# Performance work log

Measured on AMD Instinct MI355X. Metric: run time of the kernel, lower is better.

## Reference

```python
import jax, jax.numpy as jnp
import numpy as np

MARGIN = 40.0


def setup_inputs() -> dict:
    key = jax.random.key(0)
    k1, k2 = jax.random.split(key)
    feat = jax.random.normal(k1, (4096, 512), dtype=jnp.float32)
    targets = jax.random.randint(k2, (4096,), 0, 64, dtype=jnp.int64)
    return {"feat": feat, "targets": targets}


def reference(feat, targets):
    # corr: (n, n) Gram matrix of features
    corr = feat @ feat.T
    # mask[i, j] = True if same class
    mask = targets[:, None] == targets[None, :]
    big = jnp.asarray(jnp.finfo(corr.dtype).max, corr.dtype)
    # per-row min over positives, max over negatives
    corr_ap = jnp.min(jnp.where(mask, corr, big), axis=1)
    corr_an = jnp.max(jnp.where(mask, -big, corr), axis=1)
    # MarginRankingLoss(margin=40) with y = 1: mean(relu(-(ap - an) + margin))
    loss = jnp.mean(jax.nn.relu(corr_an - corr_ap + MARGIN))
    return loss
```

## Files before the change

kernel.cpp:

```cpp
#include <hip/hip_runtime.h>
#include <float.h>
#include <stdint.h>


#define N_ROWS 4096
#define D_K    512
#define BT     64
#define BK     32
#define NTB    (N_ROWS / BT)
#define NTILES (NTB * (NTB + 1) / 2)
#define MARGIN 40.0f
#define FOLD_BLOCKS 16

typedef __bf16 bf16_t;
typedef bf16_t bf16x8 __attribute__((ext_vector_type(8)));
typedef float  floatx4 __attribute__((ext_vector_type(4)));
typedef unsigned short ushort_t;
typedef ushort_t ushortx8 __attribute__((ext_vector_type(8)));

#define GLOAD_LDS16(g, l)                                        \
    __builtin_amdgcn_global_load_lds(                            \
        (const __attribute__((address_space(1))) void*)(g),      \
        (__attribute__((address_space(3))) void*)(l), 16, 0, 0)

__device__ __forceinline__ ushort_t f2bf_rne(float x) {
    uint32_t u = __builtin_bit_cast(uint32_t, x);
    return (ushort_t)((u + 0x7FFFu + ((u >> 16) & 1u)) >> 16);
}

__global__ __launch_bounds__(256) void cast_kernel(
    const float* __restrict__ f, ushort_t* __restrict__ o,
    int* __restrict__ counter)
{
    const int gid = blockIdx.x * 256 + threadIdx.x;
    if (gid == 0) *counter = 0;

    const int i = gid * 8;
    const float4 v0 = *(const float4*)(f + i);
    const float4 v1 = *(const float4*)(f + i + 4);
    ushortx8 r;
    r[0] = f2bf_rne(v0.x); r[1] = f2bf_rne(v0.y);
    r[2] = f2bf_rne(v0.z); r[3] = f2bf_rne(v0.w);
    r[4] = f2bf_rne(v1.x); r[5] = f2bf_rne(v1.y);
    r[6] = f2bf_rne(v1.z); r[7] = f2bf_rne(v1.w);
    *(ushortx8*)(o + i) = r;
}

__global__ __launch_bounds__(256) void gram_mfma_kernel(
    const ushort_t* __restrict__ fb, const int* __restrict__ tgt,
    float* __restrict__ ap_part, float* __restrict__ an_part)
{
    __shared__ __align__(16) ushort_t As[BT * BK];
    __shared__ __align__(16) ushort_t Bs[BT * BK];
    __shared__ int tgI[BT];
    __shared__ int tgJ[BT];
    __shared__ float apRed[2][BT],  anRed[2][BT];
    __shared__ float apRedT[2][BT], anRedT[2][BT];

    int bi = 0, rem = blockIdx.x;
    while (rem >= NTB - bi) { rem -= NTB - bi; ++bi; }
    const int bj = bi + rem;

    const int tid  = threadIdx.x;
    const int i0   = bi * BT;
    const int j0   = bj * BT;
    const int lane = tid & 63;
    const int wave = tid >> 6;
    const int wr   = wave >> 1;
    const int wc   = wave & 1;
    const int lr   = lane & 15;
    const int lg   = lane >> 4;

    if (tid < BT)            tgI[tid]      = tgt[i0 + tid];
    else if (tid < 2 * BT)   tgJ[tid - BT] = tgt[j0 + tid - BT];

    const int srow = tid >> 2;
    const int skq  = tid & 3;
    const size_t gA0 = (size_t)(i0 + srow) * D_K + skq * 8;
    const size_t gB0 = (size_t)(j0 + srow) * D_K + skq * 8;
    char* AsB = (char*)As;
    char* BsB = (char*)Bs;

    floatx4 acc[2][2];
#pragma unroll
    for (int a = 0; a < 2; ++a)
#pragma unroll
        for (int b = 0; b < 2; ++b) acc[a][b] = (floatx4)0.0f;

    for (int k0 = 0; k0 < D_K; k0 += BK) {
        GLOAD_LDS16(fb + gA0 + k0, AsB + tid * 16);
        GLOAD_LDS16(fb + gB0 + k0, BsB + tid * 16);
        __syncthreads();

        bf16x8 af[2], bf[2];
#pragma unroll
        for (int rg = 0; rg < 2; ++rg)
            af[rg] = *(const bf16x8*)(As + ((wr * 32 + rg * 16 + lr) * BK + lg * 8));
#pragma unroll
        for (int cg = 0; cg < 2; ++cg)
            bf[cg] = *(const bf16x8*)(Bs + ((wc * 32 + cg * 16 + lr) * BK + lg * 8));
#pragma unroll
        for (int rg = 0; rg < 2; ++rg)
#pragma unroll
            for (int cg = 0; cg < 2; ++cg)
                acc[rg][cg] = __builtin_amdgcn_mfma_f32_16x16x32_bf16(
                    af[rg], bf[cg], acc[rg][cg], 0, 0, 0);
        __syncthreads();
    }

    int tj[2];
#pragma unroll
    for (int cg = 0; cg < 2; ++cg) tj[cg] = tgJ[wc * 32 + cg * 16 + lr];

    float apT[2], anT[2];
#pragma unroll
    for (int cg = 0; cg < 2; ++cg) { apT[cg] = FLT_MAX; anT[cg] = -FLT_MAX; }

#pragma unroll
    for (int rg = 0; rg < 2; ++rg) {
#pragma unroll
        for (int r = 0; r < 4; ++r) {
            const int rloc = wr * 32 + rg * 16 + lg * 4 + r;
            const int ti = tgI[rloc];
            float vap = FLT_MAX, van = -FLT_MAX;
#pragma unroll
            for (int cg = 0; cg < 2; ++cg) {
                const float v = acc[rg][cg][r];
                if (ti == tj[cg]) { vap = fminf(vap, v); apT[cg] = fminf(apT[cg], v); }
                else              { van = fmaxf(van, v); anT[cg] = fmaxf(anT[cg], v); }
            }
#pragma unroll
            for (int m = 1; m < 16; m <<= 1) {
                vap = fminf(vap, __shfl_xor(vap, m));
                van = fmaxf(van, __shfl_xor(van, m));
            }
            if (lr == 0) { apRed[wc][rloc] = vap; anRed[wc][rloc] = van; }
        }
    }
#pragma unroll
    for (int cg = 0; cg < 2; ++cg) {
        float vap = apT[cg], van = anT[cg];
        vap = fminf(vap, __shfl_xor(vap, 16)); van = fmaxf(van, __shfl_xor(van, 16));
        vap = fminf(vap, __shfl_xor(vap, 32)); van = fmaxf(van, __shfl_xor(van, 32));
        if (lg == 0) {
            apRedT[wr][wc * 32 + cg * 16 + lr] = vap;
            anRedT[wr][wc * 32 + cg * 16 + lr] = van;
        }
    }
    __syncthreads();

    if (tid < BT) {
        ap_part[(size_t)bj * N_ROWS + i0 + tid] = fminf(apRed[0][tid], apRed[1][tid]);
        an_part[(size_t)bj * N_ROWS + i0 + tid] = fmaxf(anRed[0][tid], anRed[1][tid]);
        if (bi != bj) {
            ap_part[(size_t)bi * N_ROWS + j0 + tid] = fminf(apRedT[0][tid], apRedT[1][tid]);
            an_part[(size_t)bi * N_ROWS + j0 + tid] = fmaxf(anRedT[0][tid], anRedT[1][tid]);
        }
    }
}

__global__ __launch_bounds__(256) void fold_kernel(
    const float* __restrict__ ap_part, const float* __restrict__ an_part,
    float* __restrict__ blk_sum, int* __restrict__ counter,
    float* __restrict__ out)
{
    __shared__ float sred[4];
    const int tid = threadIdx.x;
    const int row = blockIdx.x * 256 + tid;
    const int lane = tid & 63;
    const int wave = tid >> 6;

    float ap = FLT_MAX, an = -FLT_MAX;
#pragma unroll 8
    for (int s = 0; s < NTB; ++s) {
        ap = fminf(ap, ap_part[(size_t)s * N_ROWS + row]);
        an = fmaxf(an, an_part[(size_t)s * N_ROWS + row]);
    }
    const float v = an - ap + MARGIN;
    float local = (v > 0.0f) ? v : 0.0f;
#pragma unroll
    for (int m = 32; m >= 1; m >>= 1) local += __shfl_down(local, m);
    if (lane == 0) sred[wave] = local;
    __syncthreads();

    if (tid == 0) {
        blk_sum[blockIdx.x] = sred[0] + sred[1] + sred[2] + sred[3];
        __threadfence();
        if (atomicAdd(counter, 1) == FOLD_BLOCKS - 1) {
            __threadfence();
            float s = 0.0f;
#pragma unroll
            for (int b = 0; b < FOLD_BLOCKS; ++b) s += blk_sum[b];
            out[0] = s * (1.0f / N_ROWS);
        }
    }
}

extern "C" void kernel_launch(void* const* d_in, const int* in_sizes, int n_in,
                              void* d_out, int out_size, void* d_ws, size_t ws_size,
                              hipStream_t stream)
{
    const float* feat = (const float*)d_in[0];
    const int*   tgt  = (const int*)d_in[1];

    ushort_t* fb      = (ushort_t*)d_ws;
    float*    ap_part = (float*)(fb + (size_t)N_ROWS * D_K);
    float*    an_part = ap_part + (size_t)NTB * N_ROWS;
    float*    blk_sum = an_part + (size_t)NTB * N_ROWS;
    int*      counter = (int*)(blk_sum + FOLD_BLOCKS);

    cast_kernel<<<(N_ROWS * D_K) / (256 * 8), 256, 0, stream>>>(feat, fb, counter);
    gram_mfma_kernel<<<NTILES, 256, 0, stream>>>(fb, tgt, ap_part, an_part);
    fold_kernel<<<FOLD_BLOCKS, 256, 0, stream>>>(ap_part, an_part, blk_sum,
                                                 counter, (float*)d_out);
}
```

Baseline: 94.76 us.

## Enlarge Gram tiles to 128x128 with BK=64 and XOR-swizzled LDS layout

Output tiles of the symmetric Gram kernel grow from 64x64 to 128x128 and the K step from 32 to 64, with 512 threads (8 waves, each computing a 64x32 sub-tile) per block. Global-to-LDS chunk placement is XOR-swizzled by row, and the fragment reads are swizzled to match, to avoid LDS bank conflicts on the wider rows. The goal is more MFMA work per barrier and per loaded byte, and fewer K iterations and partial rows for the fold kernel to reduce. In exchange there are far fewer blocks (528 instead of 2080), higher register and LDS use per block, and coarser load balance across CUs.

```diff
diff --git a/kernel.cpp b/kernel.cpp
--- a/kernel.cpp
+++ b/kernel.cpp
@@ -5,8 +5,8 @@
 
 #define N_ROWS 4096
 #define D_K    512
-#define BT     64
-#define BK     32
+#define BT     128
+#define BK     64
 #define NTB    (N_ROWS / BT)
 #define NTILES (NTB * (NTB + 1) / 2)
 #define MARGIN 40.0f
@@ -46,7 +46,7 @@
     *(ushortx8*)(o + i) = r;
 }
 
-__global__ __launch_bounds__(256) void gram_mfma_kernel(
+__global__ __launch_bounds__(512, 4) void gram_mfma_kernel(
     const ushort_t* __restrict__ fb, const int* __restrict__ tgt,
     float* __restrict__ ap_part, float* __restrict__ an_part)
 {
@@ -54,7 +54,7 @@
     __shared__ __align__(16) ushort_t Bs[BT * BK];
     __shared__ int tgI[BT];
     __shared__ int tgJ[BT];
-    __shared__ float apRed[2][BT],  anRed[2][BT];
+    __shared__ float apRed[4][BT],  anRed[4][BT];
     __shared__ float apRedT[2][BT], anRedT[2][BT];
 
     int bi = 0, rem = blockIdx.x;
@@ -66,45 +66,55 @@
     const int j0   = bj * BT;
     const int lane = tid & 63;
     const int wave = tid >> 6;
-    const int wr   = wave >> 1;
-    const int wc   = wave & 1;
+    const int wr   = wave >> 2;
+    const int wc   = wave & 3;
     const int lr   = lane & 15;
     const int lg   = lane >> 4;
+    const int sw   = lr & 7;
 
     if (tid < BT)            tgI[tid]      = tgt[i0 + tid];
     else if (tid < 2 * BT)   tgJ[tid - BT] = tgt[j0 + tid - BT];
 
-    const int srow = tid >> 2;
-    const int skq  = tid & 3;
-    const size_t gA0 = (size_t)(i0 + srow) * D_K + skq * 8;
-    const size_t gB0 = (size_t)(j0 + srow) * D_K + skq * 8;
+    const int srow = tid >> 3;
+    const int schk = (tid & 7) ^ (srow & 7);
+    const size_t gA0 = (size_t)(i0 + srow) * D_K + schk * 8;
+    const size_t gB0 = (size_t)(j0 + srow) * D_K + schk * 8;
+    const size_t gHi = (size_t)64 * D_K;
     char* AsB = (char*)As;
     char* BsB = (char*)Bs;
 
-    floatx4 acc[2][2];
-#pragma unroll
-    for (int a = 0; a < 2; ++a)
+    floatx4 acc[4][2];
+#pragma unroll
+    for (int a = 0; a < 4; ++a)
 #pragma unroll
         for (int b = 0; b < 2; ++b) acc[a][b] = (floatx4)0.0f;
 
     for (int k0 = 0; k0 < D_K; k0 += BK) {
-        GLOAD_LDS16(fb + gA0 + k0, AsB + tid * 16);
-        GLOAD_LDS16(fb + gB0 + k0, BsB + tid * 16);
+        GLOAD_LDS16(fb + gA0 + k0,       AsB + tid * 16);
+        GLOAD_LDS16(fb + gA0 + gHi + k0, AsB + 8192 + tid * 16);
+        GLOAD_LDS16(fb + gB0 + k0,       BsB + tid * 16);
+        GLOAD_LDS16(fb + gB0 + gHi + k0, BsB + 8192 + tid * 16);
         __syncthreads();
 
-        bf16x8 af[2], bf[2];
-#pragma unroll
-        for (int rg = 0; rg < 2; ++rg)
-            af[rg] = *(const bf16x8*)(As + ((wr * 32 + rg * 16 + lr) * BK + lg * 8));
-#pragma unroll
-        for (int cg = 0; cg < 2; ++cg)
-            bf[cg] = *(const bf16x8*)(Bs + ((wc * 32 + cg * 16 + lr) * BK + lg * 8));
-#pragma unroll
-        for (int rg = 0; rg < 2; ++rg)
+        bf16x8 af[2][4], bfr[2][2];
+#pragma unroll
+        for (int h = 0; h < 2; ++h) {
+            const int pc = ((h * 4 + lg) ^ sw) * 8;
+#pragma unroll
+            for (int rg = 0; rg < 4; ++rg)
+                af[h][rg] = *(const bf16x8*)(As + (wr * 64 + rg * 16 + lr) * BK + pc);
 #pragma unroll
             for (int cg = 0; cg < 2; ++cg)
-                acc[rg][cg] = __builtin_amdgcn_mfma_f32_16x16x32_bf16(
-                    af[rg], bf[cg], acc[rg][cg], 0, 0, 0);
+                bfr[h][cg] = *(const bf16x8*)(Bs + (wc * 32 + cg * 16 + lr) * BK + pc);
+        }
+#pragma unroll
+        for (int h = 0; h < 2; ++h)
+#pragma unroll
+            for (int rg = 0; rg < 4; ++rg)
+#pragma unroll
+                for (int cg = 0; cg < 2; ++cg)
+                    acc[rg][cg] = __builtin_amdgcn_mfma_f32_16x16x32_bf16(
+                        af[h][rg], bfr[h][cg], acc[rg][cg], 0, 0, 0);
         __syncthreads();
     }
 
@@ -117,10 +127,10 @@
     for (int cg = 0; cg < 2; ++cg) { apT[cg] = FLT_MAX; anT[cg] = -FLT_MAX; }
 
 #pragma unroll
-    for (int rg = 0; rg < 2; ++rg) {
+    for (int rg = 0; rg < 4; ++rg) {
 #pragma unroll
         for (int r = 0; r < 4; ++r) {
-            const int rloc = wr * 32 + rg * 16 + lg * 4 + r;
+            const int rloc = wr * 64 + rg * 16 + lg * 4 + r;
             const int ti = tgI[rloc];
             float vap = FLT_MAX, van = -FLT_MAX;
 #pragma unroll
@@ -150,11 +160,17 @@
     __syncthreads();
 
     if (tid < BT) {
-        ap_part[(size_t)bj * N_ROWS + i0 + tid] = fminf(apRed[0][tid], apRed[1][tid]);
-        an_part[(size_t)bj * N_ROWS + i0 + tid] = fmaxf(anRed[0][tid], anRed[1][tid]);
+        const float ap = fminf(fminf(apRed[0][tid], apRed[1][tid]),
+                               fminf(apRed[2][tid], apRed[3][tid]));
+        const float an = fmaxf(fmaxf(anRed[0][tid], anRed[1][tid]),
+                               fmaxf(anRed[2][tid], anRed[3][tid]));
+        ap_part[(size_t)bj * N_ROWS + i0 + tid] = ap;
+        an_part[(size_t)bj * N_ROWS + i0 + tid] = an;
         if (bi != bj) {
-            ap_part[(size_t)bi * N_ROWS + j0 + tid] = fminf(apRedT[0][tid], apRedT[1][tid]);
-            an_part[(size_t)bi * N_ROWS + j0 + tid] = fmaxf(anRedT[0][tid], anRedT[1][tid]);
+            ap_part[(size_t)bi * N_ROWS + j0 + tid] =
+                fminf(apRedT[0][tid], apRedT[1][tid]);
+            an_part[(size_t)bi * N_ROWS + j0 + tid] =
+                fmaxf(anRedT[0][tid], anRedT[1][tid]);
         }
     }
 }
@@ -210,7 +226,7 @@
     int*      counter = (int*)(blk_sum + FOLD_BLOCKS);
 
     cast_kernel<<<(N_ROWS * D_K) / (256 * 8), 256, 0, stream>>>(feat, fb, counter);
-    gram_mfma_kernel<<<NTILES, 256, 0, stream>>>(fb, tgt, ap_part, an_part);
+    gram_mfma_kernel<<<NTILES, 512, 0, stream>>>(fb, tgt, ap_part, an_part);
     fold_kernel<<<FOLD_BLOCKS, 256, 0, stream>>>(ap_part, an_part, blk_sum,
                                                  counter, (float*)d_out);
 }
```

Result: faster. 86.75 us (-8.4%).

## Enlarge Gram tiles to 128x128 with 32x32 MFMA and swizzled LDS

Applied to the files above, without the earlier changes.

Doubles the output tile to 128x128 and the K-slice to 64, and switches from 16x16x32 to 32x32x16 bf16 MFMA instructions with each wave computing a 64x64 sub-tile. LDS loads use an XOR swizzle on the 16-byte chunk index to avoid bank conflicts. The reduction scratch is aliased onto the A tile buffer to save LDS. The intent is to raise arithmetic intensity and cut the number of tiles and synchronisation steps. In exchange there are fewer blocks (528 instead of 2080), higher register pressure from 64 accumulators per lane, and longer shuffle reductions.

```diff
diff --git a/kernel.cpp b/kernel.cpp
--- a/kernel.cpp
+++ b/kernel.cpp
@@ -5,8 +5,9 @@
 
 #define N_ROWS 4096
 #define D_K    512
-#define BT     64
-#define BK     32
+#define BT     128
+#define BK     64
+#define NKIT   (D_K / BK)
 #define NTB    (N_ROWS / BT)
 #define NTILES (NTB * (NTB + 1) / 2)
 #define MARGIN 40.0f
@@ -14,7 +15,7 @@
 
 typedef __bf16 bf16_t;
 typedef bf16_t bf16x8 __attribute__((ext_vector_type(8)));
-typedef float  floatx4 __attribute__((ext_vector_type(4)));
+typedef float  floatx16 __attribute__((ext_vector_type(16)));
 typedef unsigned short ushort_t;
 typedef ushort_t ushortx8 __attribute__((ext_vector_type(8)));
 
@@ -46,7 +47,7 @@
     *(ushortx8*)(o + i) = r;
 }
 
-__global__ __launch_bounds__(256) void gram_mfma_kernel(
+__global__ __launch_bounds__(256, 4) void gram_mfma_kernel(
     const ushort_t* __restrict__ fb, const int* __restrict__ tgt,
     float* __restrict__ ap_part, float* __restrict__ an_part)
 {
@@ -54,8 +55,11 @@
     __shared__ __align__(16) ushort_t Bs[BT * BK];
     __shared__ int tgI[BT];
     __shared__ int tgJ[BT];
-    __shared__ float apRed[2][BT],  anRed[2][BT];
-    __shared__ float apRedT[2][BT], anRedT[2][BT];
+
+    float* apRed  = (float*)As;
+    float* anRed  = apRed  + 2 * BT;
+    float* apRedT = anRed  + 2 * BT;
+    float* anRedT = apRedT + 2 * BT;
 
     int bi = 0, rem = blockIdx.x;
     while (rem >= NTB - bi) { rem -= NTB - bi; ++bi; }
@@ -68,49 +72,52 @@
     const int wave = tid >> 6;
     const int wr   = wave >> 1;
     const int wc   = wave & 1;
-    const int lr   = lane & 15;
-    const int lg   = lane >> 4;
+    const int cl   = lane & 31;
+    const int hh   = lane >> 5;
 
     if (tid < BT)            tgI[tid]      = tgt[i0 + tid];
     else if (tid < 2 * BT)   tgJ[tid - BT] = tgt[j0 + tid - BT];
 
-    const int srow = tid >> 2;
-    const int skq  = tid & 3;
-    const size_t gA0 = (size_t)(i0 + srow) * D_K + skq * 8;
-    const size_t gB0 = (size_t)(j0 + srow) * D_K + skq * 8;
+    const int sr = tid >> 3;
+    const int sc = (tid & 7) ^ (sr & 7);
+    const size_t gA0 = (size_t)(i0 + sr) * D_K + sc * 8;
+    const size_t gB0 = (size_t)(j0 + sr) * D_K + sc * 8;
     char* AsB = (char*)As;
     char* BsB = (char*)Bs;
 
-    floatx4 acc[2][2];
+    floatx16 acc[2][2];
 #pragma unroll
     for (int a = 0; a < 2; ++a)
 #pragma unroll
-        for (int b = 0; b < 2; ++b) acc[a][b] = (floatx4)0.0f;
+        for (int b = 0; b < 2; ++b) acc[a][b] = (floatx16)0.0f;
 
     for (int k0 = 0; k0 < D_K; k0 += BK) {
-        GLOAD_LDS16(fb + gA0 + k0, AsB + tid * 16);
-        GLOAD_LDS16(fb + gB0 + k0, BsB + tid * 16);
+#pragma unroll
+        for (int p = 0; p < 4; ++p) {
+            GLOAD_LDS16(fb + gA0 + (size_t)p * 32 * D_K + k0,
+                        AsB + p * 4096 + tid * 16);
+            GLOAD_LDS16(fb + gB0 + (size_t)p * 32 * D_K + k0,
+                        BsB + p * 4096 + tid * 16);
+        }
         __syncthreads();
 
-        bf16x8 af[2], bf[2];
-#pragma unroll
-        for (int rg = 0; rg < 2; ++rg)
-            af[rg] = *(const bf16x8*)(As + ((wr * 32 + rg * 16 + lr) * BK + lg * 8));
-#pragma unroll
-        for (int cg = 0; cg < 2; ++cg)
-            bf[cg] = *(const bf16x8*)(Bs + ((wc * 32 + cg * 16 + lr) * BK + lg * 8));
-#pragma unroll
-        for (int rg = 0; rg < 2; ++rg)
-#pragma unroll
-            for (int cg = 0; cg < 2; ++cg)
-                acc[rg][cg] = __builtin_amdgcn_mfma_f32_16x16x32_bf16(
-                    af[rg], bf[cg], acc[rg][cg], 0, 0, 0);
+#pragma unroll
+        for (int s = 0; s < 4; ++s) {
+            const int pc8 = ((2 * s + hh) ^ (cl & 7)) * 8;
+            bf16x8 a0 = *(const bf16x8*)(As + (wr * 64 + cl) * BK + pc8);
+            bf16x8 a1 = *(const bf16x8*)(As + (wr * 64 + 32 + cl) * BK + pc8);
+            bf16x8 b0 = *(const bf16x8*)(Bs + (wc * 64 + cl) * BK + pc8);
+            bf16x8 b1 = *(const bf16x8*)(Bs + (wc * 64 + 32 + cl) * BK + pc8);
+            acc[0][0] = __builtin_amdgcn_mfma_f32_32x32x16_bf16(a0, b0, acc[0][0], 0, 0, 0);
+            acc[0][1] = __builtin_amdgcn_mfma_f32_32x32x16_bf16(a0, b1, acc[0][1], 0, 0, 0);
+            acc[1][0] = __builtin_amdgcn_mfma_f32_32x32x16_bf16(a1, b0, acc[1][0], 0, 0, 0);
+            acc[1][1] = __builtin_amdgcn_mfma_f32_32x32x16_bf16(a1, b1, acc[1][1], 0, 0, 0);
+        }
         __syncthreads();
     }
 
-    int tj[2];
-#pragma unroll
-    for (int cg = 0; cg < 2; ++cg) tj[cg] = tgJ[wc * 32 + cg * 16 + lr];
+    const int tj0 = tgJ[wc * 64 + cl];
+    const int tj1 = tgJ[wc * 64 + 32 + cl];
 
     float apT[2], anT[2];
 #pragma unroll
@@ -118,43 +125,51 @@
 
 #pragma unroll
     for (int rg = 0; rg < 2; ++rg) {
-#pragma unroll
-        for (int r = 0; r < 4; ++r) {
-            const int rloc = wr * 32 + rg * 16 + lg * 4 + r;
-            const int ti = tgI[rloc];
+        const int rbase = wr * 64 + rg * 32 + 4 * hh;
+#pragma unroll
+        for (int reg = 0; reg < 16; ++reg) {
+            const int row = rbase + (reg & 3) + 8 * (reg >> 2);
+            const int ti = tgI[row];
+            const float v0 = acc[rg][0][reg];
+            const float v1 = acc[rg][1][reg];
             float vap = FLT_MAX, van = -FLT_MAX;
-#pragma unroll
-            for (int cg = 0; cg < 2; ++cg) {
-                const float v = acc[rg][cg][r];
-                if (ti == tj[cg]) { vap = fminf(vap, v); apT[cg] = fminf(apT[cg], v); }
-                else              { van = fmaxf(van, v); anT[cg] = fmaxf(anT[cg], v); }
-            }
-#pragma unroll
-            for (int m = 1; m < 16; m <<= 1) {
+            if (ti == tj0) { vap = fminf(vap, v0); apT[0] = fminf(apT[0], v0); }
+            else           { van = fmaxf(van, v0); anT[0] = fmaxf(anT[0], v0); }
+            if (ti == tj1) { vap = fminf(vap, v1); apT[1] = fminf(apT[1], v1); }
+            else           { van = fmaxf(van, v1); anT[1] = fmaxf(anT[1], v1); }
+#pragma unroll
+            for (int m = 1; m < 32; m <<= 1) {
                 vap = fminf(vap, __shfl_xor(vap, m));
                 van = fmaxf(van, __shfl_xor(van, m));
             }
-            if (lr == 0) { apRed[wc][rloc] = vap; anRed[wc][rloc] = van; }
+            if (cl == 0) {
+                apRed[wc * BT + row] = vap;
+                anRed[wc * BT + row] = van;
+            }
         }
     }
 #pragma unroll
     for (int cg = 0; cg < 2; ++cg) {
         float vap = apT[cg], van = anT[cg];
-        vap = fminf(vap, __shfl_xor(vap, 16)); van = fmaxf(van, __shfl_xor(van, 16));
-        vap = fminf(vap, __shfl_xor(vap, 32)); van = fmaxf(van, __shfl_xor(van, 32));
-        if (lg == 0) {
-            apRedT[wr][wc * 32 + cg * 16 + lr] = vap;
-            anRedT[wr][wc * 32 + cg * 16 + lr] = van;
+        vap = fminf(vap, __shfl_xor(vap, 32));
+        van = fmaxf(van, __shfl_xor(van, 32));
+        if (lane < 32) {
+            apRedT[wr * BT + wc * 64 + cg * 32 + cl] = vap;
+            anRedT[wr * BT + wc * 64 + cg * 32 + cl] = van;
         }
     }
     __syncthreads();
 
     if (tid < BT) {
-        ap_part[(size_t)bj * N_ROWS + i0 + tid] = fminf(apRed[0][tid], apRed[1][tid]);
-        an_part[(size_t)bj * N_ROWS + i0 + tid] = fmaxf(anRed[0][tid], anRed[1][tid]);
+        ap_part[(size_t)bj * N_ROWS + i0 + tid] =
+            fminf(apRed[0 * BT + tid], apRed[1 * BT + tid]);
+        an_part[(size_t)bj * N_ROWS + i0 + tid] =
+            fmaxf(anRed[0 * BT + tid], anRed[1 * BT + tid]);
         if (bi != bj) {
-            ap_part[(size_t)bi * N_ROWS + j0 + tid] = fminf(apRedT[0][tid], apRedT[1][tid]);
-            an_part[(size_t)bi * N_ROWS + j0 + tid] = fmaxf(anRedT[0][tid], anRedT[1][tid]);
+            ap_part[(size_t)bi * N_ROWS + j0 + tid] =
+                fminf(apRedT[0 * BT + tid], apRedT[1 * BT + tid]);
+            an_part[(size_t)bi * N_ROWS + j0 + tid] =
+                fmaxf(anRedT[0 * BT + tid], anRedT[1 * BT + tid]);
         }
     }
 }
```

After: 90.64 us. -4.3%, faster.
